# Kernel optimization log

Hardware: AMD Instinct MI355X
Metric: run time of the kernel (lower is better)

The kernel has to match this reference:

```python
import jax, jax.numpy as jnp
import numpy as np

B, S, D = 16, 8192, 256  # batch, seq_len, feature dim (== hdims)
HDIMS, HEADS = 256, 8
NEG_BIG = 1e12


def setup_inputs() -> dict:
    key = jax.random.key(0)
    k1, k2, k3 = jax.random.split(key, 3)
    x = jax.random.normal(k1, (B, S, D), dtype=jnp.float32)
    mask = jnp.ones((B, S), dtype=jnp.bool_)
    # glorot-ish scaling for stability
    k_kernel = jax.random.normal(k2, (D, HDIMS), dtype=jnp.float32) * (1.0 / np.sqrt(D))
    o_kernel = jax.random.normal(k3, (HDIMS, HEADS), dtype=jnp.float32) * (1.0 / np.sqrt(HDIMS))
    return {"x": x, "mask": mask, "k_kernel": k_kernel, "o_kernel": o_kernel}


def reference(x, mask, k_kernel, o_kernel):
    # scores: Dense(tanh) -> Dense(heads), shape (B, S, HEADS)
    w = jnp.tanh(x @ k_kernel) @ o_kernel
    m = mask.astype(jnp.float32)[..., None]            # (B, S, 1)
    w = w - (1.0 - m) * NEG_BIG
    w = jax.nn.softmax(w, axis=1)                      # softmax over sequence
    # fused weighted-sum pooling: avoids (B,S,H,D) broadcast intermediate
    pooled = jnp.einsum('bsh,bsd->bhd', w, x)          # (B, HEADS, D)
    return pooled.reshape(x.shape[0], HEADS * HDIMS)   # (B, HEADS*HDIMS)
```

## Files before the change

kernel.cpp:

```cpp
#include <hip/hip_runtime.h>

#define S_LEN 8192
#define DIM   256
#define CHUNK 512
#define TB    64
#define NIT   8
#define NBLK  256

typedef __attribute__((ext_vector_type(8))) short          short8;
typedef __attribute__((ext_vector_type(4))) unsigned short u16x4;
typedef __attribute__((ext_vector_type(4))) unsigned int   u32x4;
typedef __attribute__((ext_vector_type(4))) float          f32x4;
typedef __attribute__((ext_vector_type(8))) __bf16         bf16x8;

static __device__ __forceinline__ unsigned short f2bf(float f){
  return __builtin_bit_cast(unsigned short, (__bf16)f);
}
static __device__ __forceinline__ unsigned pk2bf(float lo, float hi){
  return (unsigned)f2bf(lo) | ((unsigned)f2bf(hi) << 16);
}
static __device__ __forceinline__ float bf2f(unsigned short h){
  unsigned int u = ((unsigned int)h) << 16;
  return __builtin_bit_cast(float, u);
}
static __device__ __forceinline__ float fast_tanh(float x){
  float e = __expf(2.0f * x);
  return 1.0f - 2.0f / (e + 1.0f);
}
static __device__ __forceinline__ f32x4 mfma_bf16(short8 a, short8 b, f32x4 c){
  return __builtin_amdgcn_mfma_f32_16x16x32_bf16(
      __builtin_bit_cast(bf16x8, a), __builtin_bit_cast(bf16x8, b), c, 0, 0, 0);
}
static __device__ __forceinline__ void softbar(){
  asm volatile("s_waitcnt lgkmcnt(0)\n\ts_barrier" ::: "memory");
}


__global__ __launch_bounds__(512, 2) void k_main(
    const float* __restrict__ x, const int* __restrict__ mask,
    const float* __restrict__ ok, const float* __restrict__ kk,
    float* __restrict__ ACC, float* __restrict__ ML)
{
  __shared__ __align__(16) unsigned char sXB [32768];
  __shared__ __align__(16) unsigned char sXT2[65536];
  __shared__ __align__(16) unsigned char sT2 [32768];
  __shared__ __align__(16) unsigned char sOT [8*528];
  __shared__ __align__(16) unsigned char sPT [2*2304];
  __shared__ float sWSum[4][16];
  __shared__ float sMaskB[CHUNK];

  const int tid = threadIdx.x;
  const int w   = tid >> 6;
  const int l   = tid & 63;
  const int l15 = l & 15;
  const int lhi = l >> 4;
  const int bid = blockIdx.x;
  const int b   = bid >> 4;
  const int chunk0 = (bid & 15) * CHUNK;

  for (int idx = tid; idx < 8 * 256; idx += 512){
    int h = idx >> 8, k = idx & 255;
    *(unsigned short*)(sOT + h * 528 + k * 2) = f2bf(ok[k * 8 + h]);
  }
  sMaskB[tid] = mask[(size_t)b * S_LEN + chunk0 + tid] ? 0.0f : 1e12f;

  short8 aF[2][8];
  #pragma unroll
  for (int mi = 0; mi < 2; ++mi){
    int hidA = l15 + ((2*w + mi) << 4);
    #pragma unroll
    for (int k8 = 0; k8 < 8; ++k8){
      int col = (k8 << 5) + (lhi << 3);
      short8 v;
      #pragma unroll
      for (int e = 0; e < 8; ++e)
        v[e] = (short)f2bf(kk[(size_t)(col + e) * 256 + hidA]);
      aF[mi][k8] = v;
    }
  }

  const unsigned char* xb = (const unsigned char*)(x + ((size_t)b * S_LEN + chunk0) * DIM);
  const int dblk = l >> 2;

  f32x4 xr[8];
  #pragma unroll
  for (int q = 0; q < 8; ++q)
    xr[q] = *(const f32x4*)(xb + (((size_t)(8*w + q)) * DIM + 4*l) * 4);

  {
    unsigned vd[8][2];
    #pragma unroll
    for (int q = 0; q < 8; ++q){
      vd[q][0] = pk2bf(xr[q][0], xr[q][1]);
      vd[q][1] = pk2bf(xr[q][2], xr[q][3]);
    }
    #pragma unroll
    for (int q = 0; q < 8; ++q){
      int r = 8*w + q;
      int srow = r ^ (dblk & 3);
      int off = ((l & 3) * 8) ^ (((srow >> 2) & 1) << 4);
      *(uint2*)(sXB + dblk * 2048 + srow * 32 + off) = make_uint2(vd[q][0], vd[q][1]);
    }
    #pragma unroll
    for (int i = 0; i < 4; ++i){
      int hh = i >> 1;
      unsigned dwv[4];
      #pragma unroll
      for (int j = 0; j < 4; ++j){
        unsigned a = vd[2*j][hh], c = vd[2*j+1][hh];
        dwv[j] = (i & 1) ? ((a >> 16) | (c & 0xFFFF0000u)) : ((a & 0xFFFFu) | (c << 16));
      }
      int d = 4*l + i;
      int key = ((d & 3) << 1) ^ ((d >> 2) & 7);
      *(u32x4*)(sXT2 + d * 128 + ((16*w) ^ (key << 4))) = (u32x4){dwv[0],dwv[1],dwv[2],dwv[3]};
    }
  }
  #pragma unroll
  for (int q = 0; q < 8; ++q)
    xr[q] = *(const f32x4*)(xb + (((size_t)(TB + 8*w + q)) * DIM + 4*l) * 4);

  f32x4 acc3[2];
  acc3[0] = (f32x4){0.f,0.f,0.f,0.f};
  acc3[1] = acc3[0];
  float Lrun = 0.0f;

  __syncthreads();

  for (int it = 0; it < NIT; ++it){
    if (it > 0){
      const int pb = (it - 1) & 1;
      short8 aP0 = *(const short8*)(sPT + pb * 2304 + l15 * 144 + lhi * 16);
      short8 aP1 = *(const short8*)(sPT + pb * 2304 + l15 * 144 + 64 + lhi * 16);
      const unsigned char* srcX = sXT2 + pb * 32768;
      #pragma unroll
      for (int mi = 0; mi < 2; ++mi){
        int d = (2*w + mi) * 16 + l15;
        int key = ((d & 3) << 1) ^ ((d >> 2) & 7);
        const unsigned char* pd = srcX + d * 128;
        short8 b0 = *(const short8*)(pd + (((     lhi * 16)) ^ (key << 4)));
        short8 b1 = *(const short8*)(pd + (((64 + lhi * 16)) ^ (key << 4)));
        acc3[mi] = mfma_bf16(aP0, b0, acc3[mi]);
        acc3[mi] = mfma_bf16(aP1, b1, acc3[mi]);
      }
    }
    #pragma unroll
    for (int nt = 0; nt < 4; ++nt){
      int row = l15 + (nt << 4);
      f32x4 a0 = (f32x4){0.f,0.f,0.f,0.f};
      f32x4 a1 = a0;
      __builtin_amdgcn_s_setprio(1);
      #pragma unroll
      for (int k8 = 0; k8 < 8; ++k8){
        int dblkR = k8 * 2 + (lhi >> 1);
        int srowB = row ^ (dblkR & 3);
        int off = ((lhi & 1) * 16) ^ (((srowB >> 2) & 1) << 4);
        short8 bF = *(const short8*)(sXB + dblkR * 2048 + srowB * 32 + off);
        a0 = mfma_bf16(aF[0][k8], bF, a0);
        a1 = mfma_bf16(aF[1][k8], bF, a1);
      }
      __builtin_amdgcn_s_setprio(0);
      #pragma unroll
      for (int mi = 0; mi < 2; ++mi){
        f32x4 av = mi ? a1 : a0;
        u16x4 tv;
        #pragma unroll
        for (int r = 0; r < 4; ++r) tv[r] = f2bf(fast_tanh(av[r]));
        int hidb2 = ((((2*w + mi) << 4) + (lhi << 2))) * 2;
        *(u16x4*)(sT2 + row * 512 + (hidb2 ^ ((row & 7) << 4))) = tv;
      }
    }
    softbar();

    if (it + 1 < NIT){
      unsigned vd[8][2];
      #pragma unroll
      for (int q = 0; q < 8; ++q){
        vd[q][0] = pk2bf(xr[q][0], xr[q][1]);
        vd[q][1] = pk2bf(xr[q][2], xr[q][3]);
      }
      #pragma unroll
      for (int q = 0; q < 8; ++q){
        int r = 8*w + q;
        int srow = r ^ (dblk & 3);
        int off = ((l & 3) * 8) ^ (((srow >> 2) & 1) << 4);
        *(uint2*)(sXB + dblk * 2048 + srow * 32 + off) = make_uint2(vd[q][0], vd[q][1]);
      }
      unsigned char* dst = sXT2 + ((it + 1) & 1) * 32768;
      #pragma unroll
      for (int i = 0; i < 4; ++i){
        int hh = i >> 1;
        unsigned dwv[4];
        #pragma unroll
        for (int j = 0; j < 4; ++j){
          unsigned a = vd[2*j][hh], c = vd[2*j+1][hh];
          dwv[j] = (i & 1) ? ((a >> 16) | (c & 0xFFFF0000u)) : ((a & 0xFFFFu) | (c << 16));
        }
        int d = 4*l + i;
        int key = ((d & 3) << 1) ^ ((d >> 2) & 7);
        *(u32x4*)(dst + d * 128 + ((16*w) ^ (key << 4))) = (u32x4){dwv[0],dwv[1],dwv[2],dwv[3]};
      }
    }
    if (w < 4){
      int row = l15 + (w << 4);
      f32x4 a2a = (f32x4){0.f,0.f,0.f,0.f};
      f32x4 a2b = a2a;
      __builtin_amdgcn_s_setprio(1);
      #pragma unroll
      for (int k = 0; k < 4; ++k){
        int col2a = (k << 6) + (lhi << 4);
        int col2b = ((k + 4) << 6) + (lhi << 4);
        short8 aTa = *(const short8*)(sT2 + row * 512 + (col2a ^ ((row & 7) << 4)));
        short8 aTb = *(const short8*)(sT2 + row * 512 + (col2b ^ ((row & 7) << 4)));
        short8 bOa = (l15 < 8) ? *(const short8*)(sOT + l15 * 528 + col2a)
                               : (short8){0,0,0,0,0,0,0,0};
        short8 bOb = (l15 < 8) ? *(const short8*)(sOT + l15 * 528 + col2b)
                               : (short8){0,0,0,0,0,0,0,0};
        a2a = mfma_bf16(aTa, bOa, a2a);
        a2b = mfma_bf16(aTb, bOb, a2b);
      }
      __builtin_amdgcn_s_setprio(0);
      f32x4 a2 = a2a + a2b;
      int rbase = (w << 4) + (lhi << 2);
      #pragma unroll
      for (int r = 0; r < 4; ++r){
        float p = __expf(a2[r] - sMaskB[it * TB + rbase + r]);
        unsigned short pb2 = f2bf(p);
        Lrun += bf2f(pb2);
        *(unsigned short*)(sPT + (it & 1) * 2304 + l15 * 144 + (rbase + r) * 2) = pb2;
      }
    }
    if (it + 2 < NIT){
      #pragma unroll
      for (int q = 0; q < 8; ++q)
        xr[q] = *(const f32x4*)(xb + (((size_t)((it+2)*TB + 8*w + q)) * DIM + 4*l) * 4);
    }
    softbar();
  }

  {
    const int pb = (NIT - 1) & 1;
    short8 aP0 = *(const short8*)(sPT + pb * 2304 + l15 * 144 + lhi * 16);
    short8 aP1 = *(const short8*)(sPT + pb * 2304 + l15 * 144 + 64 + lhi * 16);
    const unsigned char* srcX = sXT2 + pb * 32768;
    #pragma unroll
    for (int mi = 0; mi < 2; ++mi){
      int d = (2*w + mi) * 16 + l15;
      int key = ((d & 3) << 1) ^ ((d >> 2) & 7);
      const unsigned char* pd = srcX + d * 128;
      short8 b0 = *(const short8*)(pd + (((     lhi * 16)) ^ (key << 4)));
      short8 b1 = *(const short8*)(pd + (((64 + lhi * 16)) ^ (key << 4)));
      acc3[mi] = mfma_bf16(aP0, b0, acc3[mi]);
      acc3[mi] = mfma_bf16(aP1, b1, acc3[mi]);
    }
  }

  if (lhi < 2){
    #pragma unroll
    for (int mi = 0; mi < 2; ++mi){
      int d = ((2*w + mi) << 4) + l15;
      #pragma unroll
      for (int r = 0; r < 4; ++r){
        int h = (lhi << 2) + r;
        ACC[((size_t)bid * 8 + h) * 256 + d] = acc3[mi][r];
      }
    }
  }
  if (w < 4){
    Lrun += __shfl_xor(Lrun, 16);
    Lrun += __shfl_xor(Lrun, 32);
    if (l < 16) sWSum[w][l] = Lrun;
  }
  __syncthreads();
  if (tid < 8)
    ML[bid * 8 + tid] = sWSum[0][tid] + sWSum[1][tid] + sWSum[2][tid] + sWSum[3][tid];
}

__global__ void k_merge(const float* __restrict__ ACC, const float* __restrict__ ML,
                        float* __restrict__ out){
  int b = blockIdx.x >> 3;
  int h = blockIdx.x & 7;
  int d = threadIdx.x;
  float L = 0.0f, V = 0.0f;
  #pragma unroll 4
  for (int c = 0; c < 16; ++c){
    int blk = b * 16 + c;
    L += ML[blk * 8 + h];
    V += ACC[((size_t)blk * 8 + h) * 256 + d];
  }
  out[(size_t)b * 2048 + h * 256 + d] = V / L;
}

extern "C" void kernel_launch(void* const* d_in, const int* in_sizes, int n_in,
                              void* d_out, int out_size, void* d_ws, size_t ws_size,
                              hipStream_t stream){
  const float* x   = (const float*)d_in[0];
  const int*  mask = (const int*) d_in[1];
  const float* kk  = (const float*)d_in[2];
  const float* ok  = (const float*)d_in[3];
  float* out = (float*)d_out;

  float* ACC = (float*)d_ws;
  float* ML  = (float*)((char*)d_ws + 2097152);

  k_main <<<NBLK, 512, 0, stream>>>(x, mask, ok, kk, ACC, ML);
  k_merge<<<128, 256, 0, stream>>>(ACC, ML, out);
}
```

Before: 53.03 us.

## Add dedicated producer waves for x loading and bf16 staging

Grows the block from 8 to 12 waves. The four new waves only load x from global memory, convert it to bf16 and write the swizzled LDS tiles for the next iteration, while the original 8 waves do only the MFMA compute. This is a warp-specialised producer/consumer split meant to take global-load latency and conversion work off the compute waves' critical path. In exchange the per-SM register budget is tighter under launch_bounds(768,3), and LDS use may limit residency to fewer blocks than the bound requests.

```diff
diff --git a/kernel.cpp b/kernel.cpp
--- a/kernel.cpp
+++ b/kernel.cpp
@@ -36,7 +36,7 @@
 }
 
 
-__global__ __launch_bounds__(512, 2) void k_main(
+__global__ __launch_bounds__(768, 3) void k_main(
     const float* __restrict__ x, const int* __restrict__ mask,
     const float* __restrict__ ok, const float* __restrict__ kk,
     float* __restrict__ ACC, float* __restrict__ ML)
@@ -58,148 +58,124 @@
   const int b   = bid >> 4;
   const int chunk0 = (bid & 15) * CHUNK;
 
-  for (int idx = tid; idx < 8 * 256; idx += 512){
+  for (int idx = tid; idx < 8 * 256; idx += 768){
     int h = idx >> 8, k = idx & 255;
     *(unsigned short*)(sOT + h * 528 + k * 2) = f2bf(ok[k * 8 + h]);
   }
-  sMaskB[tid] = mask[(size_t)b * S_LEN + chunk0 + tid] ? 0.0f : 1e12f;
-
-  short8 aF[2][8];
-  #pragma unroll
-  for (int mi = 0; mi < 2; ++mi){
-    int hidA = l15 + ((2*w + mi) << 4);
-    #pragma unroll
-    for (int k8 = 0; k8 < 8; ++k8){
-      int col = (k8 << 5) + (lhi << 3);
-      short8 v;
-      #pragma unroll
-      for (int e = 0; e < 8; ++e)
-        v[e] = (short)f2bf(kk[(size_t)(col + e) * 256 + hidA]);
-      aF[mi][k8] = v;
-    }
-  }
+  if (tid < CHUNK)
+    sMaskB[tid] = mask[(size_t)b * S_LEN + chunk0 + tid] ? 0.0f : 1e12f;
 
   const unsigned char* xb = (const unsigned char*)(x + ((size_t)b * S_LEN + chunk0) * DIM);
   const int dblk = l >> 2;
-
-  f32x4 xr[8];
-  #pragma unroll
-  for (int q = 0; q < 8; ++q)
-    xr[q] = *(const f32x4*)(xb + (((size_t)(8*w + q)) * DIM + 4*l) * 4);
-
-  {
-    unsigned vd[8][2];
-    #pragma unroll
-    for (int q = 0; q < 8; ++q){
-      vd[q][0] = pk2bf(xr[q][0], xr[q][1]);
-      vd[q][1] = pk2bf(xr[q][2], xr[q][3]);
-    }
-    #pragma unroll
-    for (int q = 0; q < 8; ++q){
-      int r = 8*w + q;
-      int srow = r ^ (dblk & 3);
-      int off = ((l & 3) * 8) ^ (((srow >> 2) & 1) << 4);
-      *(uint2*)(sXB + dblk * 2048 + srow * 32 + off) = make_uint2(vd[q][0], vd[q][1]);
-    }
-    #pragma unroll
-    for (int i = 0; i < 4; ++i){
-      int hh = i >> 1;
-      unsigned dwv[4];
-      #pragma unroll
-      for (int j = 0; j < 4; ++j){
-        unsigned a = vd[2*j][hh], c = vd[2*j+1][hh];
-        dwv[j] = (i & 1) ? ((a >> 16) | (c & 0xFFFF0000u)) : ((a & 0xFFFFu) | (c << 16));
-      }
-      int d = 4*l + i;
-      int key = ((d & 3) << 1) ^ ((d >> 2) & 7);
-      *(u32x4*)(sXT2 + d * 128 + ((16*w) ^ (key << 4))) = (u32x4){dwv[0],dwv[1],dwv[2],dwv[3]};
-    }
-  }
-  #pragma unroll
-  for (int q = 0; q < 8; ++q)
-    xr[q] = *(const f32x4*)(xb + (((size_t)(TB + 8*w + q)) * DIM + 4*l) * 4);
-
+  const int g = w - 8;
+
+  short8 aF[2][8];
   f32x4 acc3[2];
   acc3[0] = (f32x4){0.f,0.f,0.f,0.f};
   acc3[1] = acc3[0];
   float Lrun = 0.0f;
+  unsigned vd[16][2];
+
+  if (w < 8){
+    #pragma unroll
+    for (int mi = 0; mi < 2; ++mi){
+      int hidA = l15 + ((2*w + mi) << 4);
+      #pragma unroll
+      for (int k8 = 0; k8 < 8; ++k8){
+        int col = (k8 << 5) + (lhi << 3);
+        short8 v;
+        #pragma unroll
+        for (int e = 0; e < 8; ++e)
+          v[e] = (short)f2bf(kk[(size_t)(col + e) * 256 + hidA]);
+        aF[mi][k8] = v;
+      }
+    }
+  } else {
+    #pragma unroll
+    for (int q = 0; q < 16; ++q){
+      f32x4 t = *(const f32x4*)(xb + (((size_t)(16*g + q)) * DIM + 4*l) * 4);
+      vd[q][0] = pk2bf(t[0], t[1]);
+      vd[q][1] = pk2bf(t[2], t[3]);
+    }
+    #pragma unroll
+    for (int q = 0; q < 16; ++q){
+      int r = 16*g + q;
+      int srow = r ^ (dblk & 3);
+      int off = ((l & 3) * 8) ^ (((srow >> 2) & 1) << 4);
+      *(uint2*)(sXB + dblk * 2048 + srow * 32 + off) = make_uint2(vd[q][0], vd[q][1]);
+    }
+    #pragma unroll
+    for (int i = 0; i < 4; ++i){
+      int hh = i >> 1;
+      unsigned dwv[8];
+      #pragma unroll
+      for (int j = 0; j < 8; ++j){
+        unsigned a = vd[2*j][hh], c = vd[2*j+1][hh];
+        dwv[j] = (i & 1) ? ((a >> 16) | (c & 0xFFFF0000u)) : ((a & 0xFFFFu) | (c << 16));
+      }
+      int d = 4*l + i;
+      int key = ((d & 3) << 1) ^ ((d >> 2) & 7);
+      *(u32x4*)(sXT2 + d * 128 + ((32*g     ) ^ (key << 4))) = (u32x4){dwv[0],dwv[1],dwv[2],dwv[3]};
+      *(u32x4*)(sXT2 + d * 128 + ((32*g + 16) ^ (key << 4))) = (u32x4){dwv[4],dwv[5],dwv[6],dwv[7]};
+    }
+  }
 
   __syncthreads();
 
   for (int it = 0; it < NIT; ++it){
-    if (it > 0){
-      const int pb = (it - 1) & 1;
-      short8 aP0 = *(const short8*)(sPT + pb * 2304 + l15 * 144 + lhi * 16);
-      short8 aP1 = *(const short8*)(sPT + pb * 2304 + l15 * 144 + 64 + lhi * 16);
-      const unsigned char* srcX = sXT2 + pb * 32768;
-      #pragma unroll
-      for (int mi = 0; mi < 2; ++mi){
-        int d = (2*w + mi) * 16 + l15;
-        int key = ((d & 3) << 1) ^ ((d >> 2) & 7);
-        const unsigned char* pd = srcX + d * 128;
-        short8 b0 = *(const short8*)(pd + (((     lhi * 16)) ^ (key << 4)));
-        short8 b1 = *(const short8*)(pd + (((64 + lhi * 16)) ^ (key << 4)));
-        acc3[mi] = mfma_bf16(aP0, b0, acc3[mi]);
-        acc3[mi] = mfma_bf16(aP1, b1, acc3[mi]);
-      }
-    }
-    #pragma unroll
-    for (int nt = 0; nt < 4; ++nt){
-      int row = l15 + (nt << 4);
-      f32x4 a0 = (f32x4){0.f,0.f,0.f,0.f};
-      f32x4 a1 = a0;
-      __builtin_amdgcn_s_setprio(1);
-      #pragma unroll
-      for (int k8 = 0; k8 < 8; ++k8){
-        int dblkR = k8 * 2 + (lhi >> 1);
-        int srowB = row ^ (dblkR & 3);
-        int off = ((lhi & 1) * 16) ^ (((srowB >> 2) & 1) << 4);
-        short8 bF = *(const short8*)(sXB + dblkR * 2048 + srowB * 32 + off);
-        a0 = mfma_bf16(aF[0][k8], bF, a0);
-        a1 = mfma_bf16(aF[1][k8], bF, a1);
-      }
-      __builtin_amdgcn_s_setprio(0);
-      #pragma unroll
-      for (int mi = 0; mi < 2; ++mi){
-        f32x4 av = mi ? a1 : a0;
-        u16x4 tv;
-        #pragma unroll
-        for (int r = 0; r < 4; ++r) tv[r] = f2bf(fast_tanh(av[r]));
-        int hidb2 = ((((2*w + mi) << 4) + (lhi << 2))) * 2;
-        *(u16x4*)(sT2 + row * 512 + (hidb2 ^ ((row & 7) << 4))) = tv;
+    if (w < 8){
+      if (it > 0){
+        const int pb = (it - 1) & 1;
+        short8 aP0 = *(const short8*)(sPT + pb * 2304 + l15 * 144 + lhi * 16);
+        short8 aP1 = *(const short8*)(sPT + pb * 2304 + l15 * 144 + 64 + lhi * 16);
+        const unsigned char* srcX = sXT2 + pb * 32768;
+        #pragma unroll
+        for (int mi = 0; mi < 2; ++mi){
+          int d = (2*w + mi) * 16 + l15;
+          int key = ((d & 3) << 1) ^ ((d >> 2) & 7);
+          const unsigned char* pd = srcX + d * 128;
+          short8 b0 = *(const short8*)(pd + (((     lhi * 16)) ^ (key << 4)));
+          short8 b1 = *(const short8*)(pd + (((64 + lhi * 16)) ^ (key << 4)));
+          acc3[mi] = mfma_bf16(aP0, b0, acc3[mi]);
+          acc3[mi] = mfma_bf16(aP1, b1, acc3[mi]);
+        }
+      }
+      #pragma unroll
+      for (int nt = 0; nt < 4; ++nt){
+        int row = l15 + (nt << 4);
+        f32x4 a0 = (f32x4){0.f,0.f,0.f,0.f};
+        f32x4 a1 = a0;
+        __builtin_amdgcn_s_setprio(1);
+        #pragma unroll
+        for (int k8 = 0; k8 < 8; ++k8){
+          int dblkR = k8 * 2 + (lhi >> 1);
+          int srowB = row ^ (dblkR & 3);
+          int off = ((lhi & 1) * 16) ^ (((srowB >> 2) & 1) << 4);
+          short8 bF = *(const short8*)(sXB + dblkR * 2048 + srowB * 32 + off);
+          a0 = mfma_bf16(aF[0][k8], bF, a0);
+          a1 = mfma_bf16(aF[1][k8], bF, a1);
+        }
+        __builtin_amdgcn_s_setprio(0);
+        #pragma unroll
+        for (int mi = 0; mi < 2; ++mi){
+          f32x4 av = mi ? a1 : a0;
+          u16x4 tv;
+          #pragma unroll
+          for (int r = 0; r < 4; ++r) tv[r] = f2bf(fast_tanh(av[r]));
+          int hidb2 = ((((2*w + mi) << 4) + (lhi << 2))) * 2;
+          *(u16x4*)(sT2 + row * 512 + (hidb2 ^ ((row & 7) << 4))) = tv;
+        }
+      }
+    } else if (it + 1 < NIT){
+      #pragma unroll
+      for (int q = 0; q < 16; ++q){
+        f32x4 t = *(const f32x4*)(xb + (((size_t)((it+1)*TB + 16*g + q)) * DIM + 4*l) * 4);
+        vd[q][0] = pk2bf(t[0], t[1]);
+        vd[q][1] = pk2bf(t[2], t[3]);
       }
     }
     softbar();
 
-    if (it + 1 < NIT){
-      unsigned vd[8][2];
-      #pragma unroll
-      for (int q = 0; q < 8; ++q){
-        vd[q][0] = pk2bf(xr[q][0], xr[q][1]);
-        vd[q][1] = pk2bf(xr[q][2], xr[q][3]);
-      }
-      #pragma unroll
-      for (int q = 0; q < 8; ++q){
-        int r = 8*w + q;
-        int srow = r ^ (dblk & 3);
-        int off = ((l & 3) * 8) ^ (((srow >> 2) & 1) << 4);
-        *(uint2*)(sXB + dblk * 2048 + srow * 32 + off) = make_uint2(vd[q][0], vd[q][1]);
-      }
-      unsigned char* dst = sXT2 + ((it + 1) & 1) * 32768;
-      #pragma unroll
-      for (int i = 0; i < 4; ++i){
-        int hh = i >> 1;
-        unsigned dwv[4];
-        #pragma unroll
-        for (int j = 0; j < 4; ++j){
-          unsigned a = vd[2*j][hh], c = vd[2*j+1][hh];
-          dwv[j] = (i & 1) ? ((a >> 16) | (c & 0xFFFF0000u)) : ((a & 0xFFFFu) | (c << 16));
-        }
-        int d = 4*l + i;
-        int key = ((d & 3) << 1) ^ ((d >> 2) & 7);
-        *(u32x4*)(dst + d * 128 + ((16*w) ^ (key << 4))) = (u32x4){dwv[0],dwv[1],dwv[2],dwv[3]};
-      }
-    }
     if (w < 4){
       int row = l15 + (w << 4);
       f32x4 a2a = (f32x4){0.f,0.f,0.f,0.f};
@@ -228,16 +204,34 @@
         Lrun += bf2f(pb2);
         *(unsigned short*)(sPT + (it & 1) * 2304 + l15 * 144 + (rbase + r) * 2) = pb2;
       }
-    }
-    if (it + 2 < NIT){
-      #pragma unroll
-      for (int q = 0; q < 8; ++q)
-        xr[q] = *(const f32x4*)(xb + (((size_t)((it+2)*TB + 8*w + q)) * DIM + 4*l) * 4);
+    } else if (w >= 8 && it + 1 < NIT){
+      #pragma unroll
+      for (int q = 0; q < 16; ++q){
+        int r = 16*g + q;
+        int srow = r ^ (dblk & 3);
+        int off = ((l & 3) * 8) ^ (((srow >> 2) & 1) << 4);
+        *(uint2*)(sXB + dblk * 2048 + srow * 32 + off) = make_uint2(vd[q][0], vd[q][1]);
+      }
+      unsigned char* dst = sXT2 + ((it + 1) & 1) * 32768;
+      #pragma unroll
+      for (int i = 0; i < 4; ++i){
+        int hh = i >> 1;
+        unsigned dwv[8];
+        #pragma unroll
+        for (int j = 0; j < 8; ++j){
+          unsigned a = vd[2*j][hh], c = vd[2*j+1][hh];
+          dwv[j] = (i & 1) ? ((a >> 16) | (c & 0xFFFF0000u)) : ((a & 0xFFFFu) | (c << 16));
+        }
+        int d = 4*l + i;
+        int key = ((d & 3) << 1) ^ ((d >> 2) & 7);
+        *(u32x4*)(dst + d * 128 + ((32*g     ) ^ (key << 4))) = (u32x4){dwv[0],dwv[1],dwv[2],dwv[3]};
+        *(u32x4*)(dst + d * 128 + ((32*g + 16) ^ (key << 4))) = (u32x4){dwv[4],dwv[5],dwv[6],dwv[7]};
+      }
     }
     softbar();
   }
 
-  {
+  if (w < 8){
     const int pb = (NIT - 1) & 1;
     short8 aP0 = *(const short8*)(sPT + pb * 2304 + l15 * 144 + lhi * 16);
     short8 aP1 = *(const short8*)(sPT + pb * 2304 + l15 * 144 + 64 + lhi * 16);
@@ -254,7 +248,7 @@
     }
   }
 
-  if (lhi < 2){
+  if (w < 8 && lhi < 2){
     #pragma unroll
     for (int mi = 0; mi < 2; ++mi){
       int d = ((2*w + mi) << 4) + l15;
@@ -302,6 +296,6 @@
   float* ACC = (float*)d_ws;
   float* ML  = (float*)((char*)d_ws + 2097152);
 
-  k_main <<<NBLK, 512, 0, stream>>>(x, mask, ok, kk, ACC, ML);
+  k_main <<<NBLK, 768, 0, stream>>>(x, mask, ok, kk, ACC, ML);
   k_merge<<<128, 256, 0, stream>>>(ACC, ML, out);
 }
```

After: 92.91 us. +75.2%, slower.
